# Kernel tuning notes

Measured on AMD Instinct MI355X. Metric: run time of the kernel, lower is better.

## Reference

```python
import jax, jax.numpy as jnp
import numpy as np

QK_C = 64
VX_C = 128

def conv1x1(x, W, b):
    # x: [B,C,H,W], W: [O,C], b: [O] -> [B,O,H,W]
    return jnp.einsum('bchw,oc->bohw', x, W) + b[None, :, None, None]

def setup_inputs() -> dict:
    key = jax.random.key(0)
    ks = jax.random.split(key, 9)
    B, H, W = 4, 64, 64
    x = jax.random.normal(ks[0], (B, QK_C, H, W), dtype=jnp.float32)
    x_h = jax.random.normal(ks[1], (B, VX_C, H, W), dtype=jnp.float32)
    qc = QK_C // 4
    s_qk = 1.0 / np.sqrt(QK_C)
    s_v = 1.0 / np.sqrt(VX_C)
    Wq = jax.random.normal(ks[2], (qc, QK_C), dtype=jnp.float32) * s_qk
    bq = jax.random.normal(ks[3], (qc,), dtype=jnp.float32) * 0.01
    Wk = jax.random.normal(ks[4], (qc, QK_C), dtype=jnp.float32) * s_qk
    bk = jax.random.normal(ks[5], (qc,), dtype=jnp.float32) * 0.01
    Wv = jax.random.normal(ks[6], (VX_C, VX_C), dtype=jnp.float32) * s_v
    bv = jax.random.normal(ks[7], (VX_C,), dtype=jnp.float32) * 0.01
    # gamma initialized to zero in the torch module; use a small nonzero value
    # so the attention branch actually contributes to the output/gradients.
    gamma = jnp.array([0.1], dtype=jnp.float32)
    return {"x": x, "x_h": x_h, "Wq": Wq, "bq": bq, "Wk": Wk, "bk": bk,
            "Wv": Wv, "bv": bv, "gamma": gamma}

def reference(x, x_h, Wq, bq, Wk, bk, Wv, bv, gamma):
    B, C, H, W = x_h.shape
    b, c, h, w = x.shape
    N = h * w
    # 1x1-conv projections, flattened over spatial positions
    q = conv1x1(x, Wq, bq).reshape(b, -1, N)          # [B, qc, N]
    k = conv1x1(x, Wk, bk).reshape(b, -1, N)          # [B, qc, N]
    v = conv1x1(x_h, Wv, bv).reshape(B, C, H * W)     # [B, C, N]
    # energy[b, i, j] = <q[:, i], k[:, j]>
    energy = jnp.einsum('bdi,bdj->bij', q, k)          # [B, N, N]
    attention = jax.nn.softmax(energy, axis=-1)
    # out[b, c, i] = sum_j v[b, c, j] * attention[b, i, j]
    out = jnp.einsum('bcj,bij->bci', v, attention)     # [B, C, N]
    out = out.reshape(B, C, H, W)
    return gamma[0] * out + x_h
```

## Files before the change

kernel.cpp:

```cpp
#include <hip/hip_runtime.h>

#define BB 4
#define NN 4096
#define CQK 64
#define DQ 16
#define CV 128

typedef __attribute__((ext_vector_type(8))) short bf16x8;
typedef __attribute__((ext_vector_type(4))) float f32x4;
typedef __attribute__((ext_vector_type(16))) float f32x16;
typedef __attribute__((ext_vector_type(8))) unsigned short u16x8;

__device__ __forceinline__ unsigned short f2bf(float f) {
    unsigned int u = __builtin_bit_cast(unsigned int, f);
    u += 0x7FFFu + ((u >> 16) & 1u);
    return (unsigned short)(u >> 16);
}
__device__ __forceinline__ unsigned int pk_trunc(float lo, float hi) {
    unsigned int a = __builtin_bit_cast(unsigned int, lo);
    unsigned int b = __builtin_bit_cast(unsigned int, hi);
    return (a >> 16) | (b & 0xFFFF0000u);
}

__global__ __launch_bounds__(256, 4) void proj(
    const float* __restrict__ x,
    const float* __restrict__ Wq, const float* __restrict__ bq,
    const float* __restrict__ Wk, const float* __restrict__ bk,
    const float* __restrict__ xh,
    const float* __restrict__ Wv, const float* __restrict__ bv,
    unsigned short* __restrict__ qT, unsigned short* __restrict__ kT,
    unsigned short* __restrict__ vB)
{
    __shared__ __align__(16) float smem[8448];
    int tid = threadIdx.x;
    if (blockIdx.x < 512) {
        float* wvT = smem;
        float* xs  = smem + 4224;
        float* bvs = smem + 8320;
        int pt = blockIdx.x >> 1, h = blockIdx.x & 1;
        int i0 = pt * 64;
        int b = i0 >> 12, ib = i0 & 4095;
        int co0 = h * 64;
        if (tid < 64) bvs[tid] = bv[co0 + tid];
        int cog = tid & 31, ig = tid >> 5;
        float acc[8][2];
#pragma unroll
        for (int q = 0; q < 8; q++) { acc[q][0] = 0.f; acc[q][1] = 0.f; }

        for (int ch = 0; ch < 2; ch++) {
            for (int t = tid; t < 4096; t += 256) {
                int c = t & 63, col = t >> 6;
                wvT[c * 66 + col] = Wv[(size_t)(co0 + col) * CV + ch * 64 + c];
            }
            for (int t = tid; t < 4096; t += 256) {
                int il = t & 63, c = t >> 6;
                xs[c * 64 + il] = xh[((size_t)b * CV + ch * 64 + c) * NN + ib + il];
            }
            __syncthreads();
            for (int c = 0; c < 64; c++) {
                float2 w2 = *(const float2*)&wvT[c * 66 + cog * 2];
                float4 xa = *(const float4*)&xs[c * 64 + ig * 8];
                float4 xb = *(const float4*)&xs[c * 64 + ig * 8 + 4];
                float xv[8] = { xa.x, xa.y, xa.z, xa.w, xb.x, xb.y, xb.z, xb.w };
#pragma unroll
                for (int q = 0; q < 8; q++) {
                    acc[q][0] += xv[q] * w2.x;
                    acc[q][1] += xv[q] * w2.y;
                }
            }
            __syncthreads();
        }
        int kt = ib >> 6;
        int chunk = ig >> 2, quad = ig & 3;
#pragma unroll
        for (int cc = 0; cc < 2; cc++) {
            int co = co0 + cog * 2 + cc;
            int n = co >> 4, cl = co & 15;
            float bb = bvs[cog * 2 + cc];
            u16x8 o;
#pragma unroll
            for (int jj = 0; jj < 8; jj++) o[jj] = f2bf(acc[jj][cc] + bb);
            size_t base = ((size_t)(b * 64 + kt)) * 8192
                        + (size_t)(((chunk * 8 + n) * 64 + quad * 16 + cl)) * 8;
            *(u16x8*)(vB + base) = o;
        }
    } else {
        float* wqT = smem;
        float* wkT = smem + 1024;
        float* bqs = smem + 2048;
        float* bks = smem + 2064;
        for (int t = tid; t < 1024; t += 256) {
            int c = t & 63, d = t >> 6;
            wqT[c * 16 + d] = Wq[d * CQK + c];
            wkT[c * 16 + d] = Wk[d * CQK + c];
        }
        if (tid < DQ) { bqs[tid] = bq[tid]; bks[tid] = bk[tid]; }
        __syncthreads();

        int gidx = (blockIdx.x - 512) * 256 + tid;
        int b = gidx >> 12, i = gidx & 4095;
        float qa[DQ], ka[DQ];
#pragma unroll
        for (int d = 0; d < DQ; d++) { qa[d] = bqs[d]; ka[d] = bks[d]; }
        const float* xp = x + (size_t)b * CQK * NN + i;
        for (int c = 0; c < CQK; c++) {
            float xv = xp[(size_t)c * NN];
            const float4* wq4 = (const float4*)&wqT[c * DQ];
            const float4* wk4 = (const float4*)&wkT[c * DQ];
#pragma unroll
            for (int dd = 0; dd < 4; dd++) {
                float4 a = wq4[dd], e = wk4[dd];
                qa[dd*4+0] += a.x * xv; qa[dd*4+1] += a.y * xv;
                qa[dd*4+2] += a.z * xv; qa[dd*4+3] += a.w * xv;
                ka[dd*4+0] += e.x * xv; ka[dd*4+1] += e.y * xv;
                ka[dd*4+2] += e.z * xv; ka[dd*4+3] += e.w * xv;
            }
        }
        u16x8 q0, q1, k0, k1;
#pragma unroll
        for (int dd = 0; dd < 8; dd++) {
            q0[dd] = f2bf(qa[dd]);     q1[dd] = f2bf(qa[8 + dd]);
            k0[dd] = f2bf(ka[dd]);     k1[dd] = f2bf(ka[8 + dd]);
        }
        u16x8* qo = (u16x8*)(qT + (size_t)gidx * DQ);
        u16x8* ko = (u16x8*)(kT + (size_t)gidx * DQ);
        qo[0] = q0; qo[1] = q1;
        ko[0] = k0; ko[1] = k1;
    }
}

__global__ __launch_bounds__(256, 2) void flash_mfma(
    const unsigned short* __restrict__ qTb,
    const unsigned short* __restrict__ kTb,
    const unsigned short* __restrict__ vB,
    const float* __restrict__ xh,
    const float* __restrict__ gamma,
    float* __restrict__ out)
{
    __shared__ __align__(16) unsigned short pT[4 * 32 * 76];
    __shared__ __align__(16) float accs[128 * 36];
    __shared__ float l_s[4 * 2 * 32];

    int tid = threadIdx.x;
    int w = tid >> 6, lane = tid & 63;
    int q32 = lane & 31, half = lane >> 5;
    int quad = lane >> 4, cl = lane & 15;
    int b = blockIdx.x >> 7;
    int i0 = (blockIdx.x & 127) * 32;
    const f32x4 zf = {0.f, 0.f, 0.f, 0.f};
    f32x16 zf16;
#pragma unroll
    for (int r = 0; r < 16; r++) zf16[r] = 0.f;

    bf16x8 qa = *(const bf16x8*)(qTb + ((size_t)(b * NN + i0 + q32)) * DQ + half * 8);

    f32x4 acc[2][8];
#pragma unroll
    for (int g = 0; g < 2; g++)
#pragma unroll
        for (int n = 0; n < 8; n++) acc[g][n] = zf;
    float l = 0.f;

    const unsigned short* vtile = vB + ((size_t)(b * 64 + w * 16)) * 8192;
    const unsigned short* kbase = kTb + ((size_t)(b * NN + w * 16 * 64)) * DQ;
    unsigned short* pTw = pT + w * 32 * 76;

    bf16x8 kb[2], vb[16];
#pragma unroll
    for (int mg = 0; mg < 2; mg++)
        kb[mg] = *(const bf16x8*)(kbase + (size_t)(mg * 32 + q32) * DQ + half * 8);
#pragma unroll
    for (int i = 0; i < 16; i++)
        vb[i] = *(const bf16x8*)(vtile + (size_t)i * 512 + (size_t)lane * 8);

    for (int t = 0; t < 16; t++) {
        f32x16 s[2];
        s[0] = __builtin_amdgcn_mfma_f32_32x32x16_bf16(kb[0], qa, zf16, 0, 0, 0);
        s[1] = __builtin_amdgcn_mfma_f32_32x32x16_bf16(kb[1], qa, zf16, 0, 0, 0);
        const unsigned short* ktn = kbase + (size_t)(((t + 1) & 15) * 64) * DQ;
#pragma unroll
        for (int mg = 0; mg < 2; mg++)
            kb[mg] = *(const bf16x8*)(ktn + (size_t)(mg * 32 + q32) * DQ + half * 8);

#pragma unroll
        for (int mg = 0; mg < 2; mg++) {
#pragma unroll
            for (int rr = 0; rr < 4; rr++) {
                float p0 = __expf(s[mg][rr * 4 + 0]);
                float p1 = __expf(s[mg][rr * 4 + 1]);
                float p2 = __expf(s[mg][rr * 4 + 2]);
                float p3 = __expf(s[mg][rr * 4 + 3]);
                l += (p0 + p1) + (p2 + p3);
                int k0 = mg * 32 + rr * 8 + half * 4;
                *(uint2*)(pTw + q32 * 76 + k0) =
                    make_uint2(pk_trunc(p0, p1), pk_trunc(p2, p3));
            }
        }

        const unsigned short* vtn = vtile + ((t < 15) ? 8192 : 0);
#pragma unroll
        for (int ch = 0; ch < 2; ch++) {
            bf16x8 pa0 = *(const bf16x8*)(pTw + (size_t)cl * 76 + ch * 32 + quad * 8);
            bf16x8 pa1 = *(const bf16x8*)(pTw + (size_t)(16 + cl) * 76 + ch * 32 + quad * 8);
#pragma unroll
            for (int n = 0; n < 8; n++) {
                acc[0][n] = __builtin_amdgcn_mfma_f32_16x16x32_bf16(pa0, vb[ch * 8 + n], acc[0][n], 0, 0, 0);
                acc[1][n] = __builtin_amdgcn_mfma_f32_16x16x32_bf16(pa1, vb[ch * 8 + n], acc[1][n], 0, 0, 0);
            }
#pragma unroll
            for (int n = 0; n < 8; n++)
                vb[ch * 8 + n] = *(const bf16x8*)(vtn + (size_t)(ch * 8 + n) * 512 + (size_t)lane * 8);
        }
        vtile = vtn;
    }

    l_s[(w * 2 + half) * 32 + q32] = l;
    for (int ww = 0; ww < 4; ww++) {
        if (w == ww) {
#pragma unroll
            for (int g = 0; g < 2; g++)
#pragma unroll
                for (int n = 0; n < 8; n++) {
                    float* p = accs + (n * 16 + cl) * 36 + g * 16 + quad * 4;
                    if (ww == 0) *(f32x4*)p = acc[g][n];
                    else {
                        f32x4 o = *(const f32x4*)p;
                        *(f32x4*)p = o + acc[g][n];
                    }
                }
        }
        __syncthreads();
    }

    float gam = gamma[0];
    int q = tid & 31, cg = tid >> 5;
    float L = 0.f;
#pragma unroll
    for (int u = 0; u < 8; u++) L += l_s[u * 32 + q];
    float linv = 1.f / L;
#pragma unroll
    for (int cc = 0; cc < 16; cc++) {
        int c = cg * 16 + cc;
        size_t gi = ((size_t)(b * CV + c)) * NN + i0 + q;
        out[gi] = gam * accs[c * 36 + q] * linv + xh[gi];
    }
}

extern "C" void kernel_launch(void* const* d_in, const int* in_sizes, int n_in,
                              void* d_out, int out_size, void* d_ws, size_t ws_size,
                              hipStream_t stream)
{
    (void)in_sizes; (void)n_in; (void)out_size; (void)ws_size;
    const float* x  = (const float*)d_in[0];
    const float* xh = (const float*)d_in[1];
    const float* Wq = (const float*)d_in[2];
    const float* bq = (const float*)d_in[3];
    const float* Wk = (const float*)d_in[4];
    const float* bk = (const float*)d_in[5];
    const float* Wv = (const float*)d_in[6];
    const float* bv = (const float*)d_in[7];
    const float* gm = (const float*)d_in[8];
    float* out = (float*)d_out;

    char* ws = (char*)d_ws;
    unsigned short* qTb = (unsigned short*)ws;
    unsigned short* kTb = (unsigned short*)(ws + (512 << 10));
    unsigned short* vB  = (unsigned short*)(ws + (1 << 20));

    proj<<<576, 256, 0, stream>>>(x, Wq, bq, Wk, bk, xh, Wv, bv, qTb, kTb, vB);
    flash_mfma<<<BB * 128, 256, 0, stream>>>(qTb, kTb, vB, xh, gm, out);
}
```

Baseline: 122.7 us.

## Process 64 queries per block to double K/V reuse per load

Each block now handles 64 query rows instead of 32. Every K and V tile loaded from global memory is reused across twice as many queries, which halves total K/V traffic. The grid shrinks to 256 blocks, launch bounds drop to one block per SM, and accumulator registers double. The trade is lower occupancy, fewer blocks than CUs on a 256-CU part, and higher register pressure.

```diff
diff --git a/kernel.cpp b/kernel.cpp
--- a/kernel.cpp
+++ b/kernel.cpp
@@ -129,7 +129,7 @@
     }
 }
 
-__global__ __launch_bounds__(256, 2) void flash_mfma(
+__global__ __launch_bounds__(256, 1) void flash_mfma(
     const unsigned short* __restrict__ qTb,
     const unsigned short* __restrict__ kTb,
     const unsigned short* __restrict__ vB,
@@ -137,33 +137,35 @@
     const float* __restrict__ gamma,
     float* __restrict__ out)
 {
-    __shared__ __align__(16) unsigned short pT[4 * 32 * 76];
-    __shared__ __align__(16) float accs[128 * 36];
-    __shared__ float l_s[4 * 2 * 32];
+    __shared__ __align__(16) unsigned char smem[36864];
+    __shared__ float l_s[16 * 32];
 
     int tid = threadIdx.x;
     int w = tid >> 6, lane = tid & 63;
     int q32 = lane & 31, half = lane >> 5;
     int quad = lane >> 4, cl = lane & 15;
-    int b = blockIdx.x >> 7;
-    int i0 = (blockIdx.x & 127) * 32;
+    int b = blockIdx.x >> 6;
+    int i0 = (blockIdx.x & 63) * 64;
     const f32x4 zf = {0.f, 0.f, 0.f, 0.f};
     f32x16 zf16;
 #pragma unroll
     for (int r = 0; r < 16; r++) zf16[r] = 0.f;
 
-    bf16x8 qa = *(const bf16x8*)(qTb + ((size_t)(b * NN + i0 + q32)) * DQ + half * 8);
-
-    f32x4 acc[2][8];
+    bf16x8 qa[2];
 #pragma unroll
     for (int g = 0; g < 2; g++)
-#pragma unroll
-        for (int n = 0; n < 8; n++) acc[g][n] = zf;
-    float l = 0.f;
+        qa[g] = *(const bf16x8*)(qTb + ((size_t)(b * NN + i0 + g * 32 + q32)) * DQ + half * 8);
+
+    f32x4 acc[4][8];
+#pragma unroll
+    for (int gg = 0; gg < 4; gg++)
+#pragma unroll
+        for (int n = 0; n < 8; n++) acc[gg][n] = zf;
+    float l[2] = {0.f, 0.f};
 
     const unsigned short* vtile = vB + ((size_t)(b * 64 + w * 16)) * 8192;
     const unsigned short* kbase = kTb + ((size_t)(b * NN + w * 16 * 64)) * DQ;
-    unsigned short* pTw = pT + w * 32 * 76;
+    unsigned short* pTw = (unsigned short*)smem + w * 64 * 72;
 
     bf16x8 kb[2], vb[16];
 #pragma unroll
@@ -174,38 +176,46 @@
         vb[i] = *(const bf16x8*)(vtile + (size_t)i * 512 + (size_t)lane * 8);
 
     for (int t = 0; t < 16; t++) {
-        f32x16 s[2];
-        s[0] = __builtin_amdgcn_mfma_f32_32x32x16_bf16(kb[0], qa, zf16, 0, 0, 0);
-        s[1] = __builtin_amdgcn_mfma_f32_32x32x16_bf16(kb[1], qa, zf16, 0, 0, 0);
+        f32x16 s[4];
+#pragma unroll
+        for (int g = 0; g < 2; g++)
+#pragma unroll
+            for (int mg = 0; mg < 2; mg++)
+                s[g * 2 + mg] = __builtin_amdgcn_mfma_f32_32x32x16_bf16(kb[mg], qa[g], zf16, 0, 0, 0);
         const unsigned short* ktn = kbase + (size_t)(((t + 1) & 15) * 64) * DQ;
 #pragma unroll
         for (int mg = 0; mg < 2; mg++)
             kb[mg] = *(const bf16x8*)(ktn + (size_t)(mg * 32 + q32) * DQ + half * 8);
 
 #pragma unroll
-        for (int mg = 0; mg < 2; mg++) {
-#pragma unroll
-            for (int rr = 0; rr < 4; rr++) {
-                float p0 = __expf(s[mg][rr * 4 + 0]);
-                float p1 = __expf(s[mg][rr * 4 + 1]);
-                float p2 = __expf(s[mg][rr * 4 + 2]);
-                float p3 = __expf(s[mg][rr * 4 + 3]);
-                l += (p0 + p1) + (p2 + p3);
-                int k0 = mg * 32 + rr * 8 + half * 4;
-                *(uint2*)(pTw + q32 * 76 + k0) =
-                    make_uint2(pk_trunc(p0, p1), pk_trunc(p2, p3));
+        for (int g = 0; g < 2; g++) {
+#pragma unroll
+            for (int mg = 0; mg < 2; mg++) {
+#pragma unroll
+                for (int rr = 0; rr < 4; rr++) {
+                    float p0 = __expf(s[g * 2 + mg][rr * 4 + 0]);
+                    float p1 = __expf(s[g * 2 + mg][rr * 4 + 1]);
+                    float p2 = __expf(s[g * 2 + mg][rr * 4 + 2]);
+                    float p3 = __expf(s[g * 2 + mg][rr * 4 + 3]);
+                    l[g] += (p0 + p1) + (p2 + p3);
+                    *(uint2*)(pTw + (size_t)(g * 32 + q32) * 72 + mg * 32 + rr * 8 + half * 4) =
+                        make_uint2(pk_trunc(p0, p1), pk_trunc(p2, p3));
+                }
             }
         }
 
         const unsigned short* vtn = vtile + ((t < 15) ? 8192 : 0);
 #pragma unroll
         for (int ch = 0; ch < 2; ch++) {
-            bf16x8 pa0 = *(const bf16x8*)(pTw + (size_t)cl * 76 + ch * 32 + quad * 8);
-            bf16x8 pa1 = *(const bf16x8*)(pTw + (size_t)(16 + cl) * 76 + ch * 32 + quad * 8);
+            bf16x8 pa[4];
+#pragma unroll
+            for (int gg = 0; gg < 4; gg++)
+                pa[gg] = *(const bf16x8*)(pTw + (size_t)(gg * 16 + cl) * 72 + ch * 32 + quad * 8);
 #pragma unroll
             for (int n = 0; n < 8; n++) {
-                acc[0][n] = __builtin_amdgcn_mfma_f32_16x16x32_bf16(pa0, vb[ch * 8 + n], acc[0][n], 0, 0, 0);
-                acc[1][n] = __builtin_amdgcn_mfma_f32_16x16x32_bf16(pa1, vb[ch * 8 + n], acc[1][n], 0, 0, 0);
+#pragma unroll
+                for (int gg = 0; gg < 4; gg++)
+                    acc[gg][n] = __builtin_amdgcn_mfma_f32_16x16x32_bf16(pa[gg], vb[ch * 8 + n], acc[gg][n], 0, 0, 0);
             }
 #pragma unroll
             for (int n = 0; n < 8; n++)
@@ -214,18 +224,22 @@
         vtile = vtn;
     }
 
-    l_s[(w * 2 + half) * 32 + q32] = l;
+#pragma unroll
+    for (int g = 0; g < 2; g++)
+        l_s[((w * 2 + half) * 2 + g) * 32 + q32] = l[g];
+    __syncthreads();
+    float* accs = (float*)smem;
     for (int ww = 0; ww < 4; ww++) {
         if (w == ww) {
 #pragma unroll
-            for (int g = 0; g < 2; g++)
+            for (int gg = 0; gg < 4; gg++)
 #pragma unroll
                 for (int n = 0; n < 8; n++) {
-                    float* p = accs + (n * 16 + cl) * 36 + g * 16 + quad * 4;
-                    if (ww == 0) *(f32x4*)p = acc[g][n];
+                    float* p = accs + (size_t)(n * 16 + cl) * 68 + gg * 16 + quad * 4;
+                    if (ww == 0) *(f32x4*)p = acc[gg][n];
                     else {
                         f32x4 o = *(const f32x4*)p;
-                        *(f32x4*)p = o + acc[g][n];
+                        *(f32x4*)p = o + acc[gg][n];
                     }
                 }
         }
@@ -233,16 +247,17 @@
     }
 
     float gam = gamma[0];
-    int q = tid & 31, cg = tid >> 5;
+    int q = tid & 63, cgrp = tid >> 6;
+    int qg = q >> 5, qq = q & 31;
     float L = 0.f;
 #pragma unroll
-    for (int u = 0; u < 8; u++) L += l_s[u * 32 + q];
+    for (int u = 0; u < 8; u++) L += l_s[(u * 2 + qg) * 32 + qq];
     float linv = 1.f / L;
 #pragma unroll
-    for (int cc = 0; cc < 16; cc++) {
-        int c = cg * 16 + cc;
+    for (int cc = 0; cc < 32; cc++) {
+        int c = cgrp * 32 + cc;
         size_t gi = ((size_t)(b * CV + c)) * NN + i0 + q;
-        out[gi] = gam * accs[c * 36 + q] * linv + xh[gi];
+        out[gi] = gam * accs[(size_t)c * 68 + q] * linv + xh[gi];
     }
 }
 
@@ -268,5 +283,5 @@
     unsigned short* vB  = (unsigned short*)(ws + (1 << 20));
 
     proj<<<576, 256, 0, stream>>>(x, Wq, bq, Wk, bk, xh, Wv, bv, qTb, kTb, vB);
-    flash_mfma<<<BB * 128, 256, 0, stream>>>(qTb, kTb, vB, xh, gm, out);
-}
+    flash_mfma<<<BB * 64, 256, 0, stream>>>(qTb, kTb, vB, xh, gm, out);
+}
```

Measured after the change: 126.4 us. 3.0% more time.
